# Kernel tuning notes

Measured on AMD Instinct MI355X. Metric: run time of the kernel, lower is better.

The kernel has to match this reference:

```python
import jax, jax.numpy as jnp
import numpy as np
import math

N_KM = [64, 16]  # part_nums_hierarchical
SPATIAL = 891    # 11*9*9, hardcoded in the original reshape


def _make_im2cluster(C, K, seed):
    # random assignment but guarantee >=2 members per cluster (original code
    # indexes zs[0] and skips singleton clusters, but would crash on empties)
    rng = np.random.RandomState(seed)
    base = np.repeat(np.arange(K), 2)
    rest = rng.randint(0, K, size=C - base.size)
    return np.concatenate([base, rest]).astype(np.int64)


def setup_inputs() -> dict:
    key = jax.random.key(0)
    conv_features = jax.random.normal(key, (8, 4096, 11, 9, 9), dtype=jnp.float32)
    im2cluster_0 = jnp.asarray(_make_im2cluster(4096, 64, 1))
    im2cluster_1 = jnp.asarray(_make_im2cluster(4096, 16, 2))
    return {"conv_features": conv_features,
            "im2cluster_0": im2cluster_0,
            "im2cluster_1": im2cluster_1}


def _safe_norm(diff):
    # row-wise L2 norm, grad-safe at exactly-zero rows (row 0 is zs[0]-zs[0])
    sq = jnp.sum(diff * diff, axis=1)
    return jnp.where(sq > 0, jnp.sqrt(jnp.where(sq > 0, sq, 1.0)), 0.0)


def _hpro_loss(conv_features, im2clusters):
    bs, C = conv_features.shape[0], conv_features.shape[1]
    D = SPATIAL * bs
    x = conv_features.reshape(bs, C, SPATIAL)
    loss = jnp.float32(0.0)
    loss_node = jnp.float32(0.0)
    for m, K in enumerate(N_KM):
        im2c = np.asarray(im2clusters[m])  # constant indices -> concrete group sizes
        zs_m, conc_m = [], []
        for c in range(K):
            idx = np.nonzero(im2c == c)[0]
            # faithful torch reshape: [bs, n_c, 891] -> [n_c, 891*bs] (row-major)
            zs = x[:, idx, :].reshape(-1, D)
            n_c = zs.shape[0]
            norm_sum = jnp.sum(_safe_norm(zs - zs[0]))
            conc_m.append(norm_sum / (n_c * math.log(n_c + 10)))
            zs_m.append(zs)
        rs = jnp.stack([z[0] for z in zs_m], axis=1)  # [D, K] first-member reps
        for c in range(K):
            u1 = zs_m[c]
            if u1.shape[0] == 1:
                continue
            nom = jnp.sum(u1 * u1[0], axis=1) / conc_m[c]                     # [n_c]
            den = jax.scipy.special.logsumexp((u1 @ rs) / conc_m[c], axis=1)  # [n_c]
            loss = loss + (-(nom - den)).mean()
        if m == 0:
            loss_node = loss
    return loss_node / C, (loss - loss_node) / (len(N_KM) * C)


def reference(conv_features, im2cluster_0, im2cluster_1):
    return _hpro_loss(conv_features, [im2cluster_0, im2cluster_1])
```

## Files before the change

kernel.cpp:

```cpp
#include <hip/hip_runtime.h>
#include <math.h>

#define CCH 4096
#define SP 891
#define NSL 32768

typedef __attribute__((ext_vector_type(8))) short short8;
typedef __attribute__((ext_vector_type(4))) float f32x4;

__device__ __forceinline__ unsigned int pack_bf2(float a, float b) {
  unsigned int ua = __builtin_bit_cast(unsigned int, a);
  unsigned int ub = __builtin_bit_cast(unsigned int, b);
  ua = (ua + 0x7fffu + ((ua >> 16) & 1u)) >> 16;
  ub = (ub + 0x7fffu + ((ub >> 16) & 1u)) >> 16;
  return ua | (ub << 16);
}

__global__ void k_setup(const int* __restrict__ im0, const int* __restrict__ im1,
                        int* cnt0, int* off0, int* cnt1, int* off1,
                        int* mem0, int* mem1, int* rs0, int* rs1) {
  int cb = blockIdx.x;
  int level = (cb >= 64) ? 1 : 0;
  int c = level ? cb - 64 : cb;
  const int* im = level ? im1 : im0;
  int* members = level ? mem1 : mem0;
  int* rs = level ? rs1 : rs0;
  int lane = threadIdx.x;
  int lt = 0;
  for (int ch = lane; ch < CCH; ch += 64) lt += (im[ch] < c) ? 1 : 0;
  for (int o = 32; o; o >>= 1) lt += __shfl_xor(lt, o, 64);
  int base = lt;
  int cnt = 0;
  for (int chunk = 0; chunk < CCH; chunk += 64) {
    int ch = chunk + lane;
    bool m = (im[ch] == c);
    unsigned long long mk = __ballot(m);
    int pos = __popcll(mk & ((1ull << lane) - 1ull));
    if (m) members[base + cnt + pos] = ch;
    cnt += __popcll(mk);
  }
  int n = cnt;
  if (lane == 0) {
    if (level) { cnt1[c] = n; off1[c] = base; }
    else       { cnt0[c] = n; off0[c] = base; }
  }
  __syncthreads();
  for (int r = lane; r < n; r += 64) {
    #pragma unroll
    for (int q = 0; q < 8; q++) {
      int p = 8 * r + q;
      int b = p / n, j = p - b * n;
      rs[(size_t)(base + r) * 8 + q] = b * CCH + members[base + j];
    }
  }
}

__global__ void k_brep(const float* __restrict__ X,
    const int* __restrict__ off0, const int* __restrict__ off1,
    const int* __restrict__ rs0, const int* __restrict__ rs1,
    uint4* __restrict__ Bfrag0, uint4* __restrict__ Bfrag1) {
  int gid = blockIdx.x * 4 + (threadIdx.x >> 6);
  int l = threadIdx.x & 63;
  int lrow = l & 15, hi = l >> 4;
  int level = (gid >= 32) ? 1 : 0;
  int q = level ? (gid - 32) : (gid >> 2);
  int ct = level ? 0 : (gid & 3);
  int cc = ct * 16 + lrow;
  int base = level ? off1[cc] : off0[cc];
  int sid = (level ? rs1 : rs0)[(size_t)base * 8 + q];
  const float* ap = X + (size_t)sid * SP + hi * 8;
  uint4* dst = (level ? Bfrag1 + (size_t)(q * 28) * 64
                      : Bfrag0 + (size_t)((q * 4 + ct) * 28) * 64) + l;
  #pragma unroll 3
  for (int kc = 0; kc < 27; kc++) {
    float4 fa0 = *(const float4*)(ap + kc * 32);
    float4 fa1 = *(const float4*)(ap + kc * 32 + 4);
    uint4 ua;
    ua.x = pack_bf2(fa0.x, fa0.y); ua.y = pack_bf2(fa0.z, fa0.w);
    ua.z = pack_bf2(fa1.x, fa1.y); ua.w = pack_bf2(fa1.z, fa1.w);
    dst[kc * 64] = ua;
  }
  {
    float4 fa0, fa1;
    if (hi == 3) {
      fa0 = make_float4(ap[864], ap[865], ap[866], 0.f);
      fa1 = make_float4(0.f, 0.f, 0.f, 0.f);
    } else {
      fa0 = *(const float4*)(ap + 864);
      fa1 = *(const float4*)(ap + 868);
    }
    uint4 ua;
    ua.x = pack_bf2(fa0.x, fa0.y); ua.y = pack_bf2(fa0.z, fa0.w);
    ua.z = pack_bf2(fa1.x, fa1.y); ua.w = pack_bf2(fa1.z, fa1.w);
    dst[27 * 64] = ua;
  }
}

__global__ __launch_bounds__(256) void k_gemm_all(const float* __restrict__ X,
    const int* __restrict__ rs0, const int* __restrict__ rs1,
    const uint4* __restrict__ Bfrag0, const uint4* __restrict__ Bfrag1,
    float* __restrict__ P8_0, float* __restrict__ P8_1, float* __restrict__ sn2) {
  __shared__ __align__(16) unsigned short T[16 * 896];
  __shared__ int s_sid[16];
  const int q = blockIdx.y, tid = threadIdx.x;
  const int lev = blockIdx.x >> 8;
  const int rt = blockIdx.x & 255;
  const int* rs = lev ? rs1 : rs0;
  if (tid < 16) s_sid[tid] = rs[(size_t)(rt * 16 + tid) * 8 + q];
  __syncthreads();
  const int i = tid >> 4, j = tid & 15;
  const float* sp = X + (size_t)s_sid[i] * SP;
  char* Ti = (char*)(T + i * 896);
  const int isw = (i & 7) << 4;
  float s2 = 0.f;
  #pragma unroll
  for (int kcc = 0; kcc < 7; kcc++) {
    int cidx = kcc * 16 + j;
    int el = cidx * 8;
    float4 v0, v1;
    if (cidx < 111) {
      v0 = *(const float4*)(sp + el);
      v1 = *(const float4*)(sp + el + 4);
    } else {
      v0 = make_float4(sp[888], sp[889], sp[890], 0.f);
      v1 = make_float4(0.f, 0.f, 0.f, 0.f);
    }
    s2 += v0.x * v0.x + v0.y * v0.y + v0.z * v0.z + v0.w * v0.w
        + v1.x * v1.x + v1.y * v1.y + v1.z * v1.z + v1.w * v1.w;
    uint4 u;
    u.x = pack_bf2(v0.x, v0.y); u.y = pack_bf2(v0.z, v0.w);
    u.z = pack_bf2(v1.x, v1.y); u.w = pack_bf2(v1.z, v1.w);
    *(uint4*)(Ti + ((cidx * 16) ^ isw)) = u;
  }
  if (!lev) {
    s2 += __shfl_xor(s2, 1, 16); s2 += __shfl_xor(s2, 2, 16);
    s2 += __shfl_xor(s2, 4, 16); s2 += __shfl_xor(s2, 8, 16);
    if (j == 0) sn2[s_sid[i]] = s2;
  }
  __syncthreads();
  const int l = tid & 63, w = tid >> 6;
  const int lrow = l & 15, hi = l >> 4;
  const char* Abase = (const char*)T + lrow * 1792;
  const int rsw = (lrow & 7) << 4;
  if (!lev) {
    const uint4* bq = Bfrag0 + (size_t)((q * 4 + w) * 28) * 64 + l;
    f32x4 acc = {0.f, 0.f, 0.f, 0.f};
    short8 A0, A1;
    uint4 B0, B1, B2, B3;
    A0 = *(const short8*)(Abase + ((0 * 64 + hi * 16) ^ rsw));
    A1 = *(const short8*)(Abase + ((1 * 64 + hi * 16) ^ rsw));
    B0 = bq[0 * 64]; B1 = bq[1 * 64]; B2 = bq[2 * 64]; B3 = bq[3 * 64];
    #pragma unroll
    for (int kc = 0; kc < 28; kc++) {
      short8 a = (kc & 1) ? A1 : A0;
      uint4 b = (kc & 3) == 0 ? B0 : (kc & 3) == 1 ? B1 : (kc & 3) == 2 ? B2 : B3;
      acc = __builtin_amdgcn_mfma_f32_16x16x32_bf16(a, __builtin_bit_cast(short8, b), acc, 0, 0, 0);
      if (kc + 2 < 28) {
        short8 an = *(const short8*)(Abase + (((kc + 2) * 64 + hi * 16) ^ rsw));
        if (kc & 1) A1 = an; else A0 = an;
      }
      if (kc + 4 < 28) {
        uint4 bn = bq[(kc + 4) * 64];
        switch (kc & 3) { case 0: B0 = bn; break; case 1: B1 = bn; break;
                          case 2: B2 = bn; break; default: B3 = bn; }
      }
    }
    #pragma unroll
    for (int r = 0; r < 4; r++) {
      int row = rt * 16 + hi * 4 + r;
      P8_0[((size_t)q * CCH + row) * 64 + w * 16 + lrow] = acc[r];
    }
  } else {
    const uint4* bq = Bfrag1 + (size_t)(q * 28) * 64 + l;
    f32x4 acc = {0.f, 0.f, 0.f, 0.f};
    #pragma unroll
    for (int kk = 0; kk < 7; kk++) {
      int kc = w * 7 + kk;
      short8 a = *(const short8*)(Abase + ((kc * 64 + hi * 16) ^ rsw));
      uint4 b = bq[kc * 64];
      acc = __builtin_amdgcn_mfma_f32_16x16x32_bf16(a, __builtin_bit_cast(short8, b), acc, 0, 0, 0);
    }
    __syncthreads();
    float4* Tf = (float4*)T;
    Tf[w * 64 + l] = make_float4(acc[0], acc[1], acc[2], acc[3]);
    __syncthreads();
    if (w == 0) {
      float4 v0 = Tf[l], v1 = Tf[64 + l], v2 = Tf[128 + l], v3 = Tf[192 + l];
      float vr[4] = { v0.x + v1.x + v2.x + v3.x, v0.y + v1.y + v2.y + v3.y,
                      v0.z + v1.z + v2.z + v3.z, v0.w + v1.w + v2.w + v3.w };
      #pragma unroll
      for (int r = 0; r < 4; r++) {
        int row = rt * 16 + hi * 4 + r;
        P8_1[((size_t)q * CCH + row) * 16 + lrow] = vr[r];
      }
    }
  }
}

template<int K>
__device__ __forceinline__ void fin_body(const float* __restrict__ P8,
    const float* __restrict__ sn2, const int* __restrict__ rs,
    const int* __restrict__ cnt, const int* __restrict__ off,
    double* __restrict__ clLoss, int c) {
  __shared__ float pcc[4096];
  __shared__ float red[512];
  __shared__ double redd[512];
  __shared__ float s_conc;
  const int n = cnt[c], base = off[c];
  const int tid = threadIdx.x;
  float rn0 = 0.f;
  #pragma unroll
  for (int qq = 0; qq < 8; qq++) rn0 += sn2[rs[(size_t)base * 8 + qq]];
  float t = 0.f;
  for (int r = tid; r < n; r += 512) {
    float pd = 0.f, rn = 0.f;
    #pragma unroll
    for (int qq = 0; qq < 8; qq++) {
      pd += P8[((size_t)qq * CCH + base + r) * K + c];
      rn += sn2[rs[(size_t)(base + r) * 8 + qq]];
    }
    pcc[r] = pd;
    if (r > 0) {
      float d2 = rn - 2.f * pd + rn0;
      t += (d2 > 0.f) ? sqrtf(d2) : 0.f;
    }
  }
  red[tid] = t; __syncthreads();
  for (int o = 256; o; o >>= 1) { if (tid < o) red[tid] += red[tid + o]; __syncthreads(); }
  if (tid == 0) s_conc = red[0] / ((float)n * logf((float)n + 10.f));
  __syncthreads();
  const float invc = 1.f / s_conc;
  const int wv = tid >> 6, lane = tid & 63;
  const int sub = (K == 64) ? 0 : (lane >> 4);
  const int cc = lane & (K - 1);
  constexpr int RPI = 8 * (64 / K);
  double acc = 0.0;
  for (int r = wv * (64 / K) + sub; r < n; r += RPI) {
    float s = 0.f;
    #pragma unroll
    for (int qq = 0; qq < 8; qq++) s += P8[((size_t)qq * CCH + base + r) * K + cc];
    float lg = s * invc;
    float m = lg;
    #pragma unroll
    for (int o = K / 2; o; o >>= 1) m = fmaxf(m, __shfl_xor(m, o, K));
    float e = expf(lg - m);
    float se = e;
    #pragma unroll
    for (int o = K / 2; o; o >>= 1) se += __shfl_xor(se, o, K);
    if (cc == 0) acc += (double)(m + logf(se)) - (double)(pcc[r] * invc);
  }
  redd[tid] = acc; __syncthreads();
  for (int o = 256; o; o >>= 1) { if (tid < o) redd[tid] += redd[tid + o]; __syncthreads(); }
  if (tid == 0) clLoss[c] = redd[0] / (double)n;
}

__global__ __launch_bounds__(512) void k_fin_all(const float* __restrict__ P8_0,
    const float* __restrict__ P8_1, const float* __restrict__ sn2,
    const int* __restrict__ rs0, const int* __restrict__ rs1,
    const int* __restrict__ cnt0, const int* __restrict__ off0,
    const int* __restrict__ cnt1, const int* __restrict__ off1,
    double* __restrict__ cl0, double* __restrict__ cl1) {
  if (blockIdx.x < 64) fin_body<64>(P8_0, sn2, rs0, cnt0, off0, cl0, blockIdx.x);
  else                 fin_body<16>(P8_1, sn2, rs1, cnt1, off1, cl1, blockIdx.x - 64);
}

__global__ void k_final(const double* __restrict__ cl0, const double* __restrict__ cl1,
                        float* __restrict__ out) {
  if (threadIdx.x == 0) {
    double s0 = 0.0, s1 = 0.0;
    for (int i = 0; i < 64; i++) s0 += cl0[i];
    for (int i = 0; i < 16; i++) s1 += cl1[i];
    out[0] = (float)(s0 / 4096.0);
    out[1] = (float)(s1 / 8192.0);
  }
}

extern "C" void kernel_launch(void* const* d_in, const int* in_sizes, int n_in,
                              void* d_out, int out_size, void* d_ws, size_t ws_size,
                              hipStream_t stream) {
  const float* X = (const float*)d_in[0];
  const int* im0 = (const int*)d_in[1];
  const int* im1 = (const int*)d_in[2];
  float* out = (float*)d_out;

  char* w = (char*)d_ws;
  auto alloc = [&](size_t bytes) -> char* {
    char* p = w; w += (bytes + 255) & ~(size_t)255; return p;
  };
  int*    cnt0  = (int*)alloc(64 * 4);
  int*    off0  = (int*)alloc(64 * 4);
  int*    cnt1  = (int*)alloc(16 * 4);
  int*    off1  = (int*)alloc(16 * 4);
  int*    mem0  = (int*)alloc((size_t)CCH * 4);
  int*    mem1  = (int*)alloc((size_t)CCH * 4);
  int*    rs0   = (int*)alloc((size_t)CCH * 8 * 4);
  int*    rs1   = (int*)alloc((size_t)CCH * 8 * 4);
  float*  sn2   = (float*)alloc((size_t)NSL * 4);
  uint4*  Bfrag0 = (uint4*)alloc((size_t)32 * 28 * 64 * 16);
  uint4*  Bfrag1 = (uint4*)alloc((size_t)8 * 28 * 64 * 16);
  float*  P8_0  = (float*)alloc((size_t)8 * CCH * 64 * 4);
  float*  P8_1  = (float*)alloc((size_t)8 * CCH * 16 * 4);
  double* cl0   = (double*)alloc(64 * 8);
  double* cl1   = (double*)alloc(16 * 8);

  k_setup<<<80, 64, 0, stream>>>(im0, im1, cnt0, off0, cnt1, off1, mem0, mem1, rs0, rs1);
  k_brep<<<10, 256, 0, stream>>>(X, off0, off1, rs0, rs1, Bfrag0, Bfrag1);
  k_gemm_all<<<dim3(512, 8), 256, 0, stream>>>(X, rs0, rs1, Bfrag0, Bfrag1, P8_0, P8_1, sn2);
  k_fin_all<<<80, 512, 0, stream>>>(P8_0, P8_1, sn2, rs0, rs1, cnt0, off0, cnt1, off1, cl0, cl1);
  k_final<<<1, 64, 0, stream>>>(cl0, cl1, out);
}
```

Baseline: 99.02 us.

## Loop over batch slices in-block with double-buffered LDS and prefetched global loads

The GEMM kernel now launches 512 blocks instead of 512x8. Each block loops over the 8 batch slices, issuing global loads for the next slice into registers while running MFMAs on the current slice from a double-buffered LDS tile. It also replaces the XOR swizzle with row padding (904 shorts per row) and moves the level-1 reduction into a separate LDS buffer. The aim is to hide global-load latency behind compute, at the cost of fewer blocks in flight, more registers and more LDS per block.

```diff
diff --git a/kernel.cpp b/kernel.cpp
--- a/kernel.cpp
+++ b/kernel.cpp
@@ -100,63 +100,64 @@
     const int* __restrict__ rs0, const int* __restrict__ rs1,
     const uint4* __restrict__ Bfrag0, const uint4* __restrict__ Bfrag1,
     float* __restrict__ P8_0, float* __restrict__ P8_1, float* __restrict__ sn2) {
-  __shared__ __align__(16) unsigned short T[16 * 896];
-  __shared__ int s_sid[16];
-  const int q = blockIdx.y, tid = threadIdx.x;
+  __shared__ __align__(16) unsigned short T[2][16 * 904];
+  __shared__ float4 Rf[256];
+  const int tid = threadIdx.x;
   const int lev = blockIdx.x >> 8;
   const int rt = blockIdx.x & 255;
   const int* rs = lev ? rs1 : rs0;
-  if (tid < 16) s_sid[tid] = rs[(size_t)(rt * 16 + tid) * 8 + q];
-  __syncthreads();
   const int i = tid >> 4, j = tid & 15;
-  const float* sp = X + (size_t)s_sid[i] * SP;
-  char* Ti = (char*)(T + i * 896);
-  const int isw = (i & 7) << 4;
-  float s2 = 0.f;
-  #pragma unroll
-  for (int kcc = 0; kcc < 7; kcc++) {
-    int cidx = kcc * 16 + j;
-    int el = cidx * 8;
-    float4 v0, v1;
-    if (cidx < 111) {
-      v0 = *(const float4*)(sp + el);
-      v1 = *(const float4*)(sp + el + 4);
-    } else {
-      v0 = make_float4(sp[888], sp[889], sp[890], 0.f);
-      v1 = make_float4(0.f, 0.f, 0.f, 0.f);
-    }
-    s2 += v0.x * v0.x + v0.y * v0.y + v0.z * v0.z + v0.w * v0.w
-        + v1.x * v1.x + v1.y * v1.y + v1.z * v1.z + v1.w * v1.w;
-    uint4 u;
-    u.x = pack_bf2(v0.x, v0.y); u.y = pack_bf2(v0.z, v0.w);
-    u.z = pack_bf2(v1.x, v1.y); u.w = pack_bf2(v1.z, v1.w);
-    *(uint4*)(Ti + ((cidx * 16) ^ isw)) = u;
-  }
-  if (!lev) {
-    s2 += __shfl_xor(s2, 1, 16); s2 += __shfl_xor(s2, 2, 16);
-    s2 += __shfl_xor(s2, 4, 16); s2 += __shfl_xor(s2, 8, 16);
-    if (j == 0) sn2[s_sid[i]] = s2;
-  }
-  __syncthreads();
   const int l = tid & 63, w = tid >> 6;
   const int lrow = l & 15, hi = l >> 4;
-  const char* Abase = (const char*)T + lrow * 1792;
-  const int rsw = (lrow & 7) << 4;
-  if (!lev) {
-    const uint4* bq = Bfrag0 + (size_t)((q * 4 + w) * 28) * 64 + l;
+
+  float4 s0a, s0b, s1a, s1b, s2a, s2b, s3a, s3b, s4a, s4b, s5a, s5b, s6a, s6b;
+  int sidn;
+
+#define ISSUE_ALL(qq) { \
+    sidn = rs[(size_t)(rt * 16 + i) * 8 + (qq)]; \
+    const float* sp_ = X + (size_t)sidn * SP; \
+    s0a = *(const float4*)(sp_ + (0 * 16 + j) * 8); s0b = *(const float4*)(sp_ + (0 * 16 + j) * 8 + 4); \
+    s1a = *(const float4*)(sp_ + (1 * 16 + j) * 8); s1b = *(const float4*)(sp_ + (1 * 16 + j) * 8 + 4); \
+    s2a = *(const float4*)(sp_ + (2 * 16 + j) * 8); s2b = *(const float4*)(sp_ + (2 * 16 + j) * 8 + 4); \
+    s3a = *(const float4*)(sp_ + (3 * 16 + j) * 8); s3b = *(const float4*)(sp_ + (3 * 16 + j) * 8 + 4); \
+    s4a = *(const float4*)(sp_ + (4 * 16 + j) * 8); s4b = *(const float4*)(sp_ + (4 * 16 + j) * 8 + 4); \
+    s5a = *(const float4*)(sp_ + (5 * 16 + j) * 8); s5b = *(const float4*)(sp_ + (5 * 16 + j) * 8 + 4); \
+    if (j < 15) { s6a = *(const float4*)(sp_ + (6 * 16 + j) * 8); s6b = *(const float4*)(sp_ + (6 * 16 + j) * 8 + 4); } \
+    else { s6a = make_float4(sp_[888], sp_[889], sp_[890], 0.f); s6b = make_float4(0.f, 0.f, 0.f, 0.f); } }
+
+#define W1(Ti, kcc, va, vb) { \
+    uint4 u_; \
+    u_.x = pack_bf2(va.x, va.y); u_.y = pack_bf2(va.z, va.w); \
+    u_.z = pack_bf2(vb.x, vb.y); u_.w = pack_bf2(vb.z, vb.w); \
+    *(uint4*)((Ti) + ((kcc) * 16 + j) * 16) = u_; \
+    s2l += va.x * va.x + va.y * va.y + va.z * va.z + va.w * va.w \
+         + vb.x * vb.x + vb.y * vb.y + vb.z * vb.z + vb.w * vb.w; }
+
+#define WRITE_ALL(buf) { \
+    char* Ti = (char*)&T[(buf)][i * 904]; \
+    float s2l = 0.f; \
+    W1(Ti, 0, s0a, s0b) W1(Ti, 1, s1a, s1b) W1(Ti, 2, s2a, s2b) W1(Ti, 3, s3a, s3b) \
+    W1(Ti, 4, s4a, s4b) W1(Ti, 5, s5a, s5b) W1(Ti, 6, s6a, s6b) \
+    if (!lev) { \
+      s2l += __shfl_xor(s2l, 1, 16); s2l += __shfl_xor(s2l, 2, 16); \
+      s2l += __shfl_xor(s2l, 4, 16); s2l += __shfl_xor(s2l, 8, 16); \
+      if (j == 0) sn2[sidn] = s2l; \
+    } }
+
+  auto computeL0 = [&](int qq, int buf) {
+    const char* Abase = (const char*)&T[buf][0] + lrow * 1808;
+    const uint4* bq = Bfrag0 + (size_t)((qq * 4 + w) * 28) * 64 + l;
     f32x4 acc = {0.f, 0.f, 0.f, 0.f};
-    short8 A0, A1;
-    uint4 B0, B1, B2, B3;
-    A0 = *(const short8*)(Abase + ((0 * 64 + hi * 16) ^ rsw));
-    A1 = *(const short8*)(Abase + ((1 * 64 + hi * 16) ^ rsw));
-    B0 = bq[0 * 64]; B1 = bq[1 * 64]; B2 = bq[2 * 64]; B3 = bq[3 * 64];
+    short8 A0 = *(const short8*)(Abase + (0 * 64 + hi * 16));
+    short8 A1 = *(const short8*)(Abase + (1 * 64 + hi * 16));
+    uint4 B0 = bq[0 * 64], B1 = bq[1 * 64], B2 = bq[2 * 64], B3 = bq[3 * 64];
     #pragma unroll
     for (int kc = 0; kc < 28; kc++) {
       short8 a = (kc & 1) ? A1 : A0;
       uint4 b = (kc & 3) == 0 ? B0 : (kc & 3) == 1 ? B1 : (kc & 3) == 2 ? B2 : B3;
       acc = __builtin_amdgcn_mfma_f32_16x16x32_bf16(a, __builtin_bit_cast(short8, b), acc, 0, 0, 0);
       if (kc + 2 < 28) {
-        short8 an = *(const short8*)(Abase + (((kc + 2) * 64 + hi * 16) ^ rsw));
+        short8 an = *(const short8*)(Abase + ((kc + 2) * 64 + hi * 16));
         if (kc & 1) A1 = an; else A0 = an;
       }
       if (kc + 4 < 28) {
@@ -168,33 +169,51 @@
     #pragma unroll
     for (int r = 0; r < 4; r++) {
       int row = rt * 16 + hi * 4 + r;
-      P8_0[((size_t)q * CCH + row) * 64 + w * 16 + lrow] = acc[r];
-    }
-  } else {
-    const uint4* bq = Bfrag1 + (size_t)(q * 28) * 64 + l;
+      P8_0[((size_t)qq * CCH + row) * 64 + w * 16 + lrow] = acc[r];
+    }
+  };
+
+  auto computeL1 = [&](int qq, int buf) {
+    const char* Abase = (const char*)&T[buf][0] + lrow * 1808;
+    const uint4* bq = Bfrag1 + (size_t)(qq * 28) * 64 + l;
     f32x4 acc = {0.f, 0.f, 0.f, 0.f};
     #pragma unroll
     for (int kk = 0; kk < 7; kk++) {
       int kc = w * 7 + kk;
-      short8 a = *(const short8*)(Abase + ((kc * 64 + hi * 16) ^ rsw));
+      short8 a = *(const short8*)(Abase + (kc * 64 + hi * 16));
       uint4 b = bq[kc * 64];
       acc = __builtin_amdgcn_mfma_f32_16x16x32_bf16(a, __builtin_bit_cast(short8, b), acc, 0, 0, 0);
     }
     __syncthreads();
-    float4* Tf = (float4*)T;
-    Tf[w * 64 + l] = make_float4(acc[0], acc[1], acc[2], acc[3]);
+    Rf[w * 64 + l] = make_float4(acc[0], acc[1], acc[2], acc[3]);
     __syncthreads();
     if (w == 0) {
-      float4 v0 = Tf[l], v1 = Tf[64 + l], v2 = Tf[128 + l], v3 = Tf[192 + l];
+      float4 v0 = Rf[l], v1 = Rf[64 + l], v2 = Rf[128 + l], v3 = Rf[192 + l];
       float vr[4] = { v0.x + v1.x + v2.x + v3.x, v0.y + v1.y + v2.y + v3.y,
                       v0.z + v1.z + v2.z + v3.z, v0.w + v1.w + v2.w + v3.w };
       #pragma unroll
       for (int r = 0; r < 4; r++) {
         int row = rt * 16 + hi * 4 + r;
-        P8_1[((size_t)q * CCH + row) * 16 + lrow] = vr[r];
+        P8_1[((size_t)qq * CCH + row) * 16 + lrow] = vr[r];
       }
     }
-  }
+  };
+
+  ISSUE_ALL(0);
+  WRITE_ALL(0);
+  __syncthreads();
+  for (int qq = 0; qq < 8; qq++) {
+    const int buf = qq & 1;
+    if (qq < 7) ISSUE_ALL(qq + 1);
+    if (!lev) computeL0(qq, buf); else computeL1(qq, buf);
+    if (qq < 7) {
+      WRITE_ALL(buf ^ 1);
+      __syncthreads();
+    }
+  }
+#undef ISSUE_ALL
+#undef W1
+#undef WRITE_ALL
 }
 
 template<int K>
@@ -305,7 +324,7 @@
 
   k_setup<<<80, 64, 0, stream>>>(im0, im1, cnt0, off0, cnt1, off1, mem0, mem1, rs0, rs1);
   k_brep<<<10, 256, 0, stream>>>(X, off0, off1, rs0, rs1, Bfrag0, Bfrag1);
-  k_gemm_all<<<dim3(512, 8), 256, 0, stream>>>(X, rs0, rs1, Bfrag0, Bfrag1, P8_0, P8_1, sn2);
+  k_gemm_all<<<512, 256, 0, stream>>>(X, rs0, rs1, Bfrag0, Bfrag1, P8_0, P8_1, sn2);
   k_fin_all<<<80, 512, 0, stream>>>(P8_0, P8_1, sn2, rs0, rs1, cnt0, off0, cnt1, off1, cl0, cl1);
   k_final<<<1, 64, 0, stream>>>(cl0, cl1, out);
 }
```

After: 102.2 us. 1.03x slower.

## Split gemm into two kernels, staging level-1 rows as bf16 buffer

Applied to the files above, without the earlier changes.

The level-0 gemm kernel now also writes the bf16-converted rows into a staging buffer Y1, placed in level-1 order through an inverse index built in setup. A separate level-1 kernel then reads half-size bf16 rows instead of re-reading and converting fp32 input. Row loading switches to a per-wave contiguous float4 layout with padded LDS rows in place of the XOR swizzle. The cost is an extra ~58MB of bf16 writes and reads plus one more kernel launch, in exchange for avoiding a second pass over the fp32 input.

```diff
diff --git a/kernel.cpp b/kernel.cpp
--- a/kernel.cpp
+++ b/kernel.cpp
@@ -18,7 +18,7 @@
 
 __global__ void k_setup(const int* __restrict__ im0, const int* __restrict__ im1,
                         int* cnt0, int* off0, int* cnt1, int* off1,
-                        int* mem0, int* mem1, int* rs0, int* rs1) {
+                        int* mem0, int* mem1, int* rs0, int* rs1, int* inv1) {
   int cb = blockIdx.x;
   int level = (cb >= 64) ? 1 : 0;
   int c = level ? cb - 64 : cb;
@@ -50,7 +50,9 @@
     for (int q = 0; q < 8; q++) {
       int p = 8 * r + q;
       int b = p / n, j = p - b * n;
-      rs[(size_t)(base + r) * 8 + q] = b * CCH + members[base + j];
+      int sid = b * CCH + members[base + j];
+      rs[(size_t)(base + r) * 8 + q] = sid;
+      if (level) inv1[sid] = ((base + r) << 3) | q;
     }
   }
 }
@@ -96,103 +98,124 @@
   }
 }
 
-__global__ __launch_bounds__(256) void k_gemm_all(const float* __restrict__ X,
-    const int* __restrict__ rs0, const int* __restrict__ rs1,
-    const uint4* __restrict__ Bfrag0, const uint4* __restrict__ Bfrag1,
-    float* __restrict__ P8_0, float* __restrict__ P8_1, float* __restrict__ sn2) {
-  __shared__ __align__(16) unsigned short T[16 * 896];
+__global__ __launch_bounds__(256) void k_gemm0(const float* __restrict__ X,
+    const int* __restrict__ rs0, const int* __restrict__ inv1,
+    const uint4* __restrict__ Bfrag0, float* __restrict__ P8_0,
+    unsigned short* __restrict__ Y1, float* __restrict__ sn2) {
+  __shared__ __align__(16) unsigned short T[16 * 904];
   __shared__ int s_sid[16];
-  const int q = blockIdx.y, tid = threadIdx.x;
-  const int lev = blockIdx.x >> 8;
-  const int rt = blockIdx.x & 255;
-  const int* rs = lev ? rs1 : rs0;
-  if (tid < 16) s_sid[tid] = rs[(size_t)(rt * 16 + tid) * 8 + q];
-  __syncthreads();
-  const int i = tid >> 4, j = tid & 15;
-  const float* sp = X + (size_t)s_sid[i] * SP;
-  char* Ti = (char*)(T + i * 896);
-  const int isw = (i & 7) << 4;
-  float s2 = 0.f;
-  #pragma unroll
-  for (int kcc = 0; kcc < 7; kcc++) {
-    int cidx = kcc * 16 + j;
-    int el = cidx * 8;
-    float4 v0, v1;
-    if (cidx < 111) {
-      v0 = *(const float4*)(sp + el);
-      v1 = *(const float4*)(sp + el + 4);
-    } else {
-      v0 = make_float4(sp[888], sp[889], sp[890], 0.f);
-      v1 = make_float4(0.f, 0.f, 0.f, 0.f);
-    }
-    s2 += v0.x * v0.x + v0.y * v0.y + v0.z * v0.z + v0.w * v0.w
-        + v1.x * v1.x + v1.y * v1.y + v1.z * v1.z + v1.w * v1.w;
-    uint4 u;
-    u.x = pack_bf2(v0.x, v0.y); u.y = pack_bf2(v0.z, v0.w);
-    u.z = pack_bf2(v1.x, v1.y); u.w = pack_bf2(v1.z, v1.w);
-    *(uint4*)(Ti + ((cidx * 16) ^ isw)) = u;
-  }
-  if (!lev) {
-    s2 += __shfl_xor(s2, 1, 16); s2 += __shfl_xor(s2, 2, 16);
-    s2 += __shfl_xor(s2, 4, 16); s2 += __shfl_xor(s2, 8, 16);
-    if (j == 0) sn2[s_sid[i]] = s2;
-  }
-  __syncthreads();
+  const int rt = blockIdx.x, q = blockIdx.y, tid = threadIdx.x;
   const int l = tid & 63, w = tid >> 6;
   const int lrow = l & 15, hi = l >> 4;
-  const char* Abase = (const char*)T + lrow * 1792;
-  const int rsw = (lrow & 7) << 4;
-  if (!lev) {
-    const uint4* bq = Bfrag0 + (size_t)((q * 4 + w) * 28) * 64 + l;
-    f32x4 acc = {0.f, 0.f, 0.f, 0.f};
-    short8 A0, A1;
-    uint4 B0, B1, B2, B3;
-    A0 = *(const short8*)(Abase + ((0 * 64 + hi * 16) ^ rsw));
-    A1 = *(const short8*)(Abase + ((1 * 64 + hi * 16) ^ rsw));
-    B0 = bq[0 * 64]; B1 = bq[1 * 64]; B2 = bq[2 * 64]; B3 = bq[3 * 64];
-    #pragma unroll
-    for (int kc = 0; kc < 28; kc++) {
-      short8 a = (kc & 1) ? A1 : A0;
-      uint4 b = (kc & 3) == 0 ? B0 : (kc & 3) == 1 ? B1 : (kc & 3) == 2 ? B2 : B3;
-      acc = __builtin_amdgcn_mfma_f32_16x16x32_bf16(a, __builtin_bit_cast(short8, b), acc, 0, 0, 0);
-      if (kc + 2 < 28) {
-        short8 an = *(const short8*)(Abase + (((kc + 2) * 64 + hi * 16) ^ rsw));
-        if (kc & 1) A1 = an; else A0 = an;
+  if (tid < 16) s_sid[tid] = rs0[(size_t)(rt * 16 + tid) * 8 + q];
+  __syncthreads();
+  const uint4* bq = Bfrag0 + (size_t)((q * 4 + w) * 28) * 64 + l;
+  uint4 B0 = bq[0 * 64], B1 = bq[1 * 64], B2 = bq[2 * 64], B3 = bq[3 * 64];
+  float4 sv[4][4];
+  #pragma unroll
+  for (int si = 0; si < 4; si++) {
+    const float* sp = X + (size_t)s_sid[w * 4 + si] * SP;
+    #pragma unroll
+    for (int t = 0; t < 4; t++) {
+      int el = t * 256 + 4 * l;
+      float4 v;
+      if (t < 3)           v = *(const float4*)(sp + el);
+      else if (l <= 29)    v = *(const float4*)(sp + el);
+      else if (l == 30)    v = make_float4(sp[888], sp[889], sp[890], 0.f);
+      else                 v = make_float4(0.f, 0.f, 0.f, 0.f);
+      sv[si][t] = v;
+    }
+  }
+  #pragma unroll
+  for (int si = 0; si < 4; si++) {
+    int sid = s_sid[w * 4 + si];
+    float s2 = 0.f;
+    #pragma unroll
+    for (int t = 0; t < 4; t++) {
+      float4 v = sv[si][t];
+      s2 += v.x * v.x + v.y * v.y + v.z * v.z + v.w * v.w;
+    }
+    for (int o = 32; o; o >>= 1) s2 += __shfl_xor(s2, o, 64);
+    if (l == 0) sn2[sid] = s2;
+    int inv = inv1[sid];
+    unsigned short* y1 = Y1 + ((size_t)(inv & 7) * CCH + (inv >> 3)) * 896;
+    unsigned short* Trow = T + (w * 4 + si) * 904;
+    #pragma unroll
+    for (int t = 0; t < 4; t++) {
+      float4 v = sv[si][t];
+      uint2 u;
+      u.x = pack_bf2(v.x, v.y); u.y = pack_bf2(v.z, v.w);
+      if (t < 3 || l < 32) {
+        *(uint2*)(Trow + t * 256 + 4 * l) = u;
+        *(uint2*)(y1 + t * 256 + 4 * l) = u;
       }
-      if (kc + 4 < 28) {
-        uint4 bn = bq[(kc + 4) * 64];
-        switch (kc & 3) { case 0: B0 = bn; break; case 1: B1 = bn; break;
-                          case 2: B2 = bn; break; default: B3 = bn; }
-      }
-    }
+    }
+  }
+  __syncthreads();
+  const char* Abase = (const char*)T + lrow * 1808;
+  f32x4 acc = {0.f, 0.f, 0.f, 0.f};
+  short8 A0 = *(const short8*)(Abase + (0 * 64 + hi * 16));
+  short8 A1 = *(const short8*)(Abase + (1 * 64 + hi * 16));
+  #pragma unroll
+  for (int kc = 0; kc < 28; kc++) {
+    short8 a = (kc & 1) ? A1 : A0;
+    uint4 b = (kc & 3) == 0 ? B0 : (kc & 3) == 1 ? B1 : (kc & 3) == 2 ? B2 : B3;
+    acc = __builtin_amdgcn_mfma_f32_16x16x32_bf16(a, __builtin_bit_cast(short8, b), acc, 0, 0, 0);
+    if (kc + 2 < 28) {
+      short8 an = *(const short8*)(Abase + ((kc + 2) * 64 + hi * 16));
+      if (kc & 1) A1 = an; else A0 = an;
+    }
+    if (kc + 4 < 28) {
+      uint4 bn = bq[(kc + 4) * 64];
+      switch (kc & 3) { case 0: B0 = bn; break; case 1: B1 = bn; break;
+                        case 2: B2 = bn; break; default: B3 = bn; }
+    }
+  }
+  #pragma unroll
+  for (int r = 0; r < 4; r++) {
+    int row = rt * 16 + hi * 4 + r;
+    P8_0[((size_t)q * CCH + row) * 64 + w * 16 + lrow] = acc[r];
+  }
+}
+
+__global__ __launch_bounds__(256) void k_gemm1(const unsigned short* __restrict__ Y1,
+    const uint4* __restrict__ Bfrag1, float* __restrict__ P8_1) {
+  __shared__ __align__(16) unsigned short T[16 * 904];
+  __shared__ float4 Rf[256];
+  const int rt = blockIdx.x, q = blockIdx.y, tid = threadIdx.x;
+  const int l = tid & 63, w = tid >> 6;
+  const int lrow = l & 15, hi = l >> 4;
+  const uint4* bq = Bfrag1 + (size_t)(q * 28) * 64 + l;
+  #pragma unroll
+  for (int si = 0; si < 4; si++) {
+    int i = w * 4 + si;
+    const unsigned short* src = Y1 + ((size_t)q * CCH + rt * 16 + i) * 896;
+    uint4 a0 = *(const uint4*)(src + l * 8);
+    uint4 a1 = (l < 48) ? *(const uint4*)(src + 512 + l * 8) : make_uint4(0, 0, 0, 0);
+    *(uint4*)(T + i * 904 + l * 8) = a0;
+    if (l < 48) *(uint4*)(T + i * 904 + 512 + l * 8) = a1;
+  }
+  __syncthreads();
+  const char* Abase = (const char*)T + lrow * 1808;
+  f32x4 acc = {0.f, 0.f, 0.f, 0.f};
+  #pragma unroll
+  for (int kk = 0; kk < 7; kk++) {
+    int kc = w * 7 + kk;
+    short8 a = *(const short8*)(Abase + (kc * 64 + hi * 16));
+    uint4 b = bq[kc * 64];
+    acc = __builtin_amdgcn_mfma_f32_16x16x32_bf16(a, __builtin_bit_cast(short8, b), acc, 0, 0, 0);
+  }
+  __syncthreads();
+  Rf[w * 64 + l] = make_float4(acc[0], acc[1], acc[2], acc[3]);
+  __syncthreads();
+  if (w == 0) {
+    float4 v0 = Rf[l], v1 = Rf[64 + l], v2 = Rf[128 + l], v3 = Rf[192 + l];
+    float vr[4] = { v0.x + v1.x + v2.x + v3.x, v0.y + v1.y + v2.y + v3.y,
+                    v0.z + v1.z + v2.z + v3.z, v0.w + v1.w + v2.w + v3.w };
     #pragma unroll
     for (int r = 0; r < 4; r++) {
       int row = rt * 16 + hi * 4 + r;
-      P8_0[((size_t)q * CCH + row) * 64 + w * 16 + lrow] = acc[r];
-    }
-  } else {
-    const uint4* bq = Bfrag1 + (size_t)(q * 28) * 64 + l;
-    f32x4 acc = {0.f, 0.f, 0.f, 0.f};
-    #pragma unroll
-    for (int kk = 0; kk < 7; kk++) {
-      int kc = w * 7 + kk;
-      short8 a = *(const short8*)(Abase + ((kc * 64 + hi * 16) ^ rsw));
-      uint4 b = bq[kc * 64];
-      acc = __builtin_amdgcn_mfma_f32_16x16x32_bf16(a, __builtin_bit_cast(short8, b), acc, 0, 0, 0);
-    }
-    __syncthreads();
-    float4* Tf = (float4*)T;
-    Tf[w * 64 + l] = make_float4(acc[0], acc[1], acc[2], acc[3]);
-    __syncthreads();
-    if (w == 0) {
-      float4 v0 = Tf[l], v1 = Tf[64 + l], v2 = Tf[128 + l], v3 = Tf[192 + l];
-      float vr[4] = { v0.x + v1.x + v2.x + v3.x, v0.y + v1.y + v2.y + v3.y,
-                      v0.z + v1.z + v2.z + v3.z, v0.w + v1.w + v2.w + v3.w };
-      #pragma unroll
-      for (int r = 0; r < 4; r++) {
-        int row = rt * 16 + hi * 4 + r;
-        P8_1[((size_t)q * CCH + row) * 16 + lrow] = vr[r];
-      }
+      P8_1[((size_t)q * CCH + row) * 16 + lrow] = vr[r];
     }
   }
 }
@@ -295,17 +318,20 @@
   int*    mem1  = (int*)alloc((size_t)CCH * 4);
   int*    rs0   = (int*)alloc((size_t)CCH * 8 * 4);
   int*    rs1   = (int*)alloc((size_t)CCH * 8 * 4);
+  int*    inv1  = (int*)alloc((size_t)NSL * 4);
   float*  sn2   = (float*)alloc((size_t)NSL * 4);
   uint4*  Bfrag0 = (uint4*)alloc((size_t)32 * 28 * 64 * 16);
   uint4*  Bfrag1 = (uint4*)alloc((size_t)8 * 28 * 64 * 16);
+  unsigned short* Y1 = (unsigned short*)alloc((size_t)8 * CCH * 896 * 2);
   float*  P8_0  = (float*)alloc((size_t)8 * CCH * 64 * 4);
   float*  P8_1  = (float*)alloc((size_t)8 * CCH * 16 * 4);
   double* cl0   = (double*)alloc(64 * 8);
   double* cl1   = (double*)alloc(16 * 8);
 
-  k_setup<<<80, 64, 0, stream>>>(im0, im1, cnt0, off0, cnt1, off1, mem0, mem1, rs0, rs1);
+  k_setup<<<80, 64, 0, stream>>>(im0, im1, cnt0, off0, cnt1, off1, mem0, mem1, rs0, rs1, inv1);
   k_brep<<<10, 256, 0, stream>>>(X, off0, off1, rs0, rs1, Bfrag0, Bfrag1);
-  k_gemm_all<<<dim3(512, 8), 256, 0, stream>>>(X, rs0, rs1, Bfrag0, Bfrag1, P8_0, P8_1, sn2);
+  k_gemm0<<<dim3(256, 8), 256, 0, stream>>>(X, rs0, inv1, Bfrag0, P8_0, Y1, sn2);
+  k_gemm1<<<dim3(256, 8), 256, 0, stream>>>(Y1, Bfrag1, P8_1);
   k_fin_all<<<80, 512, 0, stream>>>(P8_0, P8_1, sn2, rs0, rs1, cnt0, off0, cnt1, off1, cl0, cl1);
   k_final<<<1, 64, 0, stream>>>(cl0, cl1, out);
 }
```

Measured after the change: 105.2 us. +6.3%, slower.

## Split per-cluster finalize into row-parallel kernels with atomic accumulation

Applied to the files above, without the earlier changes.

Replaces the 80-block per-cluster finalize with two row-parallel passes. The first pass computes the per-cluster concentration numerators via shared and global atomics over 256 blocks. The second pass computes the logsumexp terms per row across many blocks and accumulates the loss atomically. This is meant to fix the poor parallelism of the old finalize, where a single block walked all rows of a large cluster. In exchange it adds a memset, an extra launch, and float atomics in place of double reductions, which makes the summation order nondeterministic.

```diff
diff --git a/kernel.cpp b/kernel.cpp
--- a/kernel.cpp
+++ b/kernel.cpp
@@ -18,13 +18,15 @@
 
 __global__ void k_setup(const int* __restrict__ im0, const int* __restrict__ im1,
                         int* cnt0, int* off0, int* cnt1, int* off1,
-                        int* mem0, int* mem1, int* rs0, int* rs1) {
+                        int* mem0, int* mem1, int* rs0, int* rs1,
+                        int* rowC0, int* rowC1) {
   int cb = blockIdx.x;
   int level = (cb >= 64) ? 1 : 0;
   int c = level ? cb - 64 : cb;
   const int* im = level ? im1 : im0;
   int* members = level ? mem1 : mem0;
   int* rs = level ? rs1 : rs0;
+  int* rowC = level ? rowC1 : rowC0;
   int lane = threadIdx.x;
   int lt = 0;
   for (int ch = lane; ch < CCH; ch += 64) lt += (im[ch] < c) ? 1 : 0;
@@ -46,6 +48,7 @@
   }
   __syncthreads();
   for (int r = lane; r < n; r += 64) {
+    rowC[base + r] = c;
     #pragma unroll
     for (int q = 0; q < 8; q++) {
       int p = 8 * r + q;
@@ -197,81 +200,83 @@
   }
 }
 
-template<int K>
-__device__ __forceinline__ void fin_body(const float* __restrict__ P8,
-    const float* __restrict__ sn2, const int* __restrict__ rs,
-    const int* __restrict__ cnt, const int* __restrict__ off,
-    double* __restrict__ clLoss, int c) {
-  __shared__ float pcc[4096];
-  __shared__ float red[512];
-  __shared__ double redd[512];
-  __shared__ float s_conc;
-  const int n = cnt[c], base = off[c];
-  const int tid = threadIdx.x;
-  float rn0 = 0.f;
-  #pragma unroll
-  for (int qq = 0; qq < 8; qq++) rn0 += sn2[rs[(size_t)base * 8 + qq]];
-  float t = 0.f;
-  for (int r = tid; r < n; r += 512) {
-    float pd = 0.f, rn = 0.f;
-    #pragma unroll
-    for (int qq = 0; qq < 8; qq++) {
-      pd += P8[((size_t)qq * CCH + base + r) * K + c];
-      rn += sn2[rs[(size_t)(base + r) * 8 + qq]];
-    }
-    pcc[r] = pd;
-    if (r > 0) {
-      float d2 = rn - 2.f * pd + rn0;
-      t += (d2 > 0.f) ? sqrtf(d2) : 0.f;
-    }
-  }
-  red[tid] = t; __syncthreads();
-  for (int o = 256; o; o >>= 1) { if (tid < o) red[tid] += red[tid + o]; __syncthreads(); }
-  if (tid == 0) s_conc = red[0] / ((float)n * logf((float)n + 10.f));
-  __syncthreads();
-  const float invc = 1.f / s_conc;
-  const int wv = tid >> 6, lane = tid & 63;
-  const int sub = (K == 64) ? 0 : (lane >> 4);
-  const int cc = lane & (K - 1);
-  constexpr int RPI = 8 * (64 / K);
-  double acc = 0.0;
-  for (int r = wv * (64 / K) + sub; r < n; r += RPI) {
-    float s = 0.f;
-    #pragma unroll
-    for (int qq = 0; qq < 8; qq++) s += P8[((size_t)qq * CCH + base + r) * K + cc];
-    float lg = s * invc;
-    float m = lg;
-    #pragma unroll
-    for (int o = K / 2; o; o >>= 1) m = fmaxf(m, __shfl_xor(m, o, K));
-    float e = expf(lg - m);
-    float se = e;
-    #pragma unroll
-    for (int o = K / 2; o; o >>= 1) se += __shfl_xor(se, o, K);
-    if (cc == 0) acc += (double)(m + logf(se)) - (double)(pcc[r] * invc);
-  }
-  redd[tid] = acc; __syncthreads();
-  for (int o = 256; o; o >>= 1) { if (tid < o) redd[tid] += redd[tid + o]; __syncthreads(); }
-  if (tid == 0) clLoss[c] = redd[0] / (double)n;
-}
-
-__global__ __launch_bounds__(512) void k_fin_all(const float* __restrict__ P8_0,
+__global__ __launch_bounds__(256) void k_fin1(const float* __restrict__ P8_0,
     const float* __restrict__ P8_1, const float* __restrict__ sn2,
     const int* __restrict__ rs0, const int* __restrict__ rs1,
-    const int* __restrict__ cnt0, const int* __restrict__ off0,
-    const int* __restrict__ cnt1, const int* __restrict__ off1,
-    double* __restrict__ cl0, double* __restrict__ cl1) {
-  if (blockIdx.x < 64) fin_body<64>(P8_0, sn2, rs0, cnt0, off0, cl0, blockIdx.x);
-  else                 fin_body<16>(P8_1, sn2, rs1, cnt1, off1, cl1, blockIdx.x - 64);
-}
-
-__global__ void k_final(const double* __restrict__ cl0, const double* __restrict__ cl1,
-                        float* __restrict__ out) {
+    const int* __restrict__ off0, const int* __restrict__ off1,
+    const int* __restrict__ rowC0, const int* __restrict__ rowC1,
+    float* __restrict__ concNum) {
+  __shared__ float cl[80];
+  int tid = threadIdx.x;
+  if (tid < 80) cl[tid] = 0.f;
+  __syncthreads();
+  int level = blockIdx.x >> 7;
+  int rbase = (blockIdx.x & 127) * 32;
+  const float* P8 = level ? P8_1 : P8_0;
+  const int* rs = level ? rs1 : rs0;
+  const int* off = level ? off1 : off0;
+  const int* rowC = level ? rowC1 : rowC0;
+  int K = level ? 16 : 64;
+  int row = rbase + (tid >> 3), q = tid & 7;
+  int c = rowC[row];
+  float p = P8[((size_t)q * CCH + row) * K + c];
+  float rn = sn2[rs[(size_t)row * 8 + q]];
+  for (int o = 1; o < 8; o <<= 1) { p += __shfl_xor(p, o, 8); rn += __shfl_xor(rn, o, 8); }
+  if (q == 0) {
+    int base = off[c];
+    if (row != base) {
+      float rn0 = 0.f;
+      for (int qq = 0; qq < 8; qq++) rn0 += sn2[rs[(size_t)base * 8 + qq]];
+      float d2 = rn - 2.f * p + rn0;
+      float sv = (d2 > 0.f) ? sqrtf(d2) : 0.f;
+      atomicAdd(&cl[level * 64 + c], sv);
+    }
+  }
+  __syncthreads();
+  if (tid < 80 && cl[tid] != 0.f) atomicAdd(&concNum[tid], cl[tid]);
+}
+
+template<int K>
+__global__ __launch_bounds__(256) void k_fin2(const float* __restrict__ P8,
+    const int* __restrict__ counts, const int* __restrict__ rowC,
+    const float* __restrict__ concNum, int cbase_g,
+    float* __restrict__ lossAcc, int lidx) {
+  __shared__ float lsum;
+  if (threadIdx.x == 0) lsum = 0.f;
+  __syncthreads();
+  constexpr int RPW = 64 / K;
+  int w = threadIdx.x >> 6, lane = threadIdx.x & 63;
+  int sub = (K == 64) ? 0 : (lane >> 4);
+  int row = blockIdx.x * (4 * RPW) + w * RPW + sub;
+  int cc = lane & (K - 1);
+  int c = rowC[row];
+  int n = counts[c];
+  float conc = concNum[cbase_g + c] / ((float)n * logf((float)n + 10.f));
+  float invc = 1.f / conc;
+  float s = 0.f;
+  #pragma unroll
+  for (int q = 0; q < 8; q++) s += P8[((size_t)q * CCH + row) * K + cc];
+  float lg = s * invc;
+  float nomv = __shfl(lg, (lane & ~(K - 1)) + c, 64);
+  float m = lg;
+  #pragma unroll
+  for (int o = K / 2; o; o >>= 1) m = fmaxf(m, __shfl_xor(m, o, K));
+  float e = expf(lg - m);
+  float se = e;
+  #pragma unroll
+  for (int o = K / 2; o; o >>= 1) se += __shfl_xor(se, o, K);
+  if (cc == 0 && n >= 2) {
+    float contrib = (m + logf(se) - nomv) / (float)n;
+    atomicAdd(&lsum, contrib);
+  }
+  __syncthreads();
+  if (threadIdx.x == 0) atomicAdd(&lossAcc[lidx], lsum);
+}
+
+__global__ void k_final(const float* __restrict__ lossAcc, float* __restrict__ out) {
   if (threadIdx.x == 0) {
-    double s0 = 0.0, s1 = 0.0;
-    for (int i = 0; i < 64; i++) s0 += cl0[i];
-    for (int i = 0; i < 16; i++) s1 += cl1[i];
-    out[0] = (float)(s0 / 4096.0);
-    out[1] = (float)(s1 / 8192.0);
+    out[0] = lossAcc[0] / 4096.0f;
+    out[1] = lossAcc[1] / 8192.0f;
   }
 }
 
@@ -287,6 +292,8 @@
   auto alloc = [&](size_t bytes) -> char* {
     char* p = w; w += (bytes + 255) & ~(size_t)255; return p;
   };
+  float* concNum = (float*)alloc((80 + 2) * 4);
+  float* lossAcc = concNum + 80;
   int*    cnt0  = (int*)alloc(64 * 4);
   int*    off0  = (int*)alloc(64 * 4);
   int*    cnt1  = (int*)alloc(16 * 4);
@@ -295,17 +302,21 @@
   int*    mem1  = (int*)alloc((size_t)CCH * 4);
   int*    rs0   = (int*)alloc((size_t)CCH * 8 * 4);
   int*    rs1   = (int*)alloc((size_t)CCH * 8 * 4);
+  int*    rowC0 = (int*)alloc((size_t)CCH * 4);
+  int*    rowC1 = (int*)alloc((size_t)CCH * 4);
   float*  sn2   = (float*)alloc((size_t)NSL * 4);
   uint4*  Bfrag0 = (uint4*)alloc((size_t)32 * 28 * 64 * 16);
   uint4*  Bfrag1 = (uint4*)alloc((size_t)8 * 28 * 64 * 16);
   float*  P8_0  = (float*)alloc((size_t)8 * CCH * 64 * 4);
   float*  P8_1  = (float*)alloc((size_t)8 * CCH * 16 * 4);
-  double* cl0   = (double*)alloc(64 * 8);
-  double* cl1   = (double*)alloc(16 * 8);
-
-  k_setup<<<80, 64, 0, stream>>>(im0, im1, cnt0, off0, cnt1, off1, mem0, mem1, rs0, rs1);
+
+  hipMemsetAsync(concNum, 0, (80 + 2) * 4, stream);
+  k_setup<<<80, 64, 0, stream>>>(im0, im1, cnt0, off0, cnt1, off1,
+                                 mem0, mem1, rs0, rs1, rowC0, rowC1);
   k_brep<<<10, 256, 0, stream>>>(X, off0, off1, rs0, rs1, Bfrag0, Bfrag1);
   k_gemm_all<<<dim3(512, 8), 256, 0, stream>>>(X, rs0, rs1, Bfrag0, Bfrag1, P8_0, P8_1, sn2);
-  k_fin_all<<<80, 512, 0, stream>>>(P8_0, P8_1, sn2, rs0, rs1, cnt0, off0, cnt1, off1, cl0, cl1);
-  k_final<<<1, 64, 0, stream>>>(cl0, cl1, out);
-}
+  k_fin1<<<256, 256, 0, stream>>>(P8_0, P8_1, sn2, rs0, rs1, off0, off1, rowC0, rowC1, concNum);
+  k_fin2<64><<<CCH / 4, 256, 0, stream>>>(P8_0, cnt0, rowC0, concNum, 0, lossAcc, 0);
+  k_fin2<16><<<CCH / 16, 256, 0, stream>>>(P8_1, cnt1, rowC1, concNum, 64, lossAcc, 1);
+  k_final<<<1, 64, 0, stream>>>(lossAcc, out);
+}
```

New measurement: 116.7 us. 17.8% more time.
